# Kernel tuning notes

Measured on AMD Instinct MI355X. Metric: run time of the kernel, lower is better.

The kernel has to match this reference:

```python
import jax, jax.numpy as jnp
import numpy as np
import math

ALPHA = 0.5


def _dfrft_matrix(N: int, a: float) -> np.ndarray:
    """Candan's discrete fractional Fourier transform matrix (approx order 2),
    as used by torch-frft's dfrft. D(a) = E diag(exp(-i*pi/2*a*k)) E^T, where E
    are eigenvectors (even/odd interleaved, descending eigenvalue) of the
    S = circulant([0,1,0,...,0,1]) + diag(Re fft(s)) matrix that commutes with the DFT.
    Pure numpy; runs at trace time (constants)."""
    s = np.zeros(N)
    s[1] = 1.0
    s[-1] = 1.0
    idx = (np.arange(N)[:, None] - np.arange(N)[None, :]) % N
    S = s[idx] + np.diag(np.fft.fft(s).real)
    # odd/even decomposition matrix P (orthogonal)
    r = N // 2
    even = 1 - (N % 2)
    P = np.zeros((N, N))
    P[0, 0] = 1.0
    c = 1.0 / math.sqrt(2.0)
    for i in range(1, r - even + 1):
        P[i, i] = c
        P[i, N - i] = c
    if even:
        P[r, r] = 1.0
    for i in range(r + 1, N):
        P[i, i] = -c
        P[i, N - i] = c
    CS = P @ S @ P.T
    C2 = CS[: r + 1, : r + 1]
    S2 = CS[r + 1:, r + 1:]
    _, vc = np.linalg.eigh(C2)  # ascending -> reverse for descending order
    _, vs = np.linalg.eigh(S2)
    SC2 = (P @ np.vstack((vc, np.zeros((N - r - 1, r + 1)))))[:, ::-1]  # even evecs
    SS2 = (P @ np.vstack((np.zeros((r + 1, N - r - 1)), vs)))[:, ::-1]  # odd evecs
    if N % 2 == 0:
        E = np.zeros((N, N + 1))
        E[:, 0::2] = SC2
        E[:, 1::2] = np.hstack((SS2, np.zeros((N, 1))))
        E = np.delete(E, N - 1, axis=1)  # skip eigenvalue index N-1, keep N
    else:
        E = np.zeros((N, N))
        E[:, 0::2] = SC2
        E[:, 1::2] = SS2
    shift = 1 - (N % 2)
    k = np.concatenate((np.arange(N - 1), [N - 1 + shift]))
    f = np.exp(-1j * (np.pi / 2.0) * a * k)
    return (E * f[None, :]) @ E.T


def setup_inputs() -> dict:
    key = jax.random.key(0)
    k1, k2, k3, k4, k5 = jax.random.split(key, 5)
    B, Ci, Co, H, W = 16, 64, 64, 128, 128
    scale = 1.0 / Ci
    return {
        "x": jax.random.normal(k1, (B, Ci, H, W), jnp.float32),
        "w_r": jax.random.normal(k2, (Co, Ci), jnp.float32) * scale,
        "w_i": jax.random.normal(k3, (Co, Ci), jnp.float32) * scale,
        "b_r": jax.random.normal(k4, (Co,), jnp.float32) * scale,
        "b_i": jax.random.normal(k5, (Co,), jnp.float32) * scale,
    }


def reference(x, w_r, w_i, b_r, b_i):
    B, Ci, H, W = x.shape
    Aw = jnp.asarray(_dfrft_matrix(W, ALPHA), jnp.complex64)   # dfrft along dim=-1
    Ah = jnp.asarray(_dfrft_matrix(H, ALPHA), jnp.complex64)   # dfrft along dim=-2
    xc = x.astype(jnp.complex64)
    # forward fractional Fourier transforms
    x_ft = jnp.einsum('wv,bchv->bchw', Aw, xc)
    x_ft = jnp.einsum('hg,bcgw->bchw', Ah, x_ft)
    # 1x1 complex conv (complex weight + bias)
    wc = w_r.astype(jnp.complex64) + 1j * w_i.astype(jnp.complex64)
    bc = b_r.astype(jnp.complex64) + 1j * b_i.astype(jnp.complex64)
    out_ft = jnp.einsum('oi,bihw->bohw', wc, x_ft) + bc[None, :, None, None]
    # inverse transforms: D(-a) = conj(D(a)) since eigenvectors are real
    y = jnp.einsum('hg,bogw->bohw', jnp.conj(Ah), out_ft)
    y = jnp.einsum('wv,bohv->bohw', jnp.conj(Aw), y)
    # module returns a complex tensor; expose as stacked (real, imag)
    return jnp.stack((y.real, y.imag), axis=0)
```

## Files before the change

### kernel.cpp

```cpp
#include <hip/hip_runtime.h>
#include <cmath>
#include <cstring>
#include <vector>
#include <algorithm>


struct UV { float ur[128]; float ui[128]; };
static UV g_uv;

namespace {

constexpr int NN = 128;

void matmul_d(const std::vector<double>& A, const std::vector<double>& B,
              std::vector<double>& C, int n) {
  for (int i = 0; i < n; ++i)
    for (int j = 0; j < n; ++j) {
      double s = 0.0;
      for (int k = 0; k < n; ++k) s += A[(size_t)i*n+k] * B[(size_t)k*n+j];
      C[(size_t)i*n+j] = s;
    }
}

void jacobi_eigh(std::vector<double>& A, int n, std::vector<double>& V,
                 std::vector<double>& lam) {
  V.assign((size_t)n*n, 0.0);
  for (int i = 0; i < n; ++i) V[(size_t)i*n+i] = 1.0;
  for (int sweep = 0; sweep < 200; ++sweep) {
    double off = 0.0;
    for (int p = 0; p < n; ++p)
      for (int q = p+1; q < n; ++q) off += A[(size_t)p*n+q]*A[(size_t)p*n+q];
    if (off < 1e-24) break;
    for (int p = 0; p < n-1; ++p)
      for (int q = p+1; q < n; ++q) {
        double apq = A[(size_t)p*n+q];
        if (std::fabs(apq) < 1e-300) continue;
        double app = A[(size_t)p*n+p], aqq = A[(size_t)q*n+q];
        double tau = (aqq - app) / (2.0*apq);
        double t = (tau >= 0 ? 1.0 : -1.0) / (std::fabs(tau) + std::sqrt(1.0 + tau*tau));
        double c = 1.0/std::sqrt(1.0 + t*t), s = t*c;
        for (int k = 0; k < n; ++k) {
          double akp = A[(size_t)k*n+p], akq = A[(size_t)k*n+q];
          A[(size_t)k*n+p] = c*akp - s*akq;
          A[(size_t)k*n+q] = s*akp + c*akq;
        }
        for (int k = 0; k < n; ++k) {
          double apk = A[(size_t)p*n+k], aqk = A[(size_t)q*n+k];
          A[(size_t)p*n+k] = c*apk - s*aqk;
          A[(size_t)q*n+k] = s*apk + c*aqk;
        }
        for (int k = 0; k < n; ++k) {
          double vkp = V[(size_t)k*n+p], vkq = V[(size_t)k*n+q];
          V[(size_t)k*n+p] = c*vkp - s*vkq;
          V[(size_t)k*n+q] = s*vkp + c*vkq;
        }
      }
  }
  lam.resize(n);
  for (int i = 0; i < n; ++i) lam[i] = A[(size_t)i*n+i];
}

bool init_uv() {
  const int n = NN, r = NN/2;
  const double c = 1.0/std::sqrt(2.0);
  const double PI = 3.14159265358979323846;
  std::vector<double> S((size_t)n*n, 0.0), P((size_t)n*n, 0.0);
  for (int i = 0; i < n; ++i) {
    S[(size_t)i*n+i] = 2.0*std::cos(2.0*PI*i/n);
    S[(size_t)i*n + (i+1)%n] += 1.0;
    S[(size_t)i*n + (i-1+n)%n] += 1.0;
  }
  P[0] = 1.0;
  for (int i = 1; i <= r-1; ++i) { P[(size_t)i*n+i] = c;  P[(size_t)i*n + (n-i)] = c; }
  P[(size_t)r*n+r] = 1.0;
  for (int i = r+1; i < n; ++i)  { P[(size_t)i*n+i] = -c; P[(size_t)i*n + (n-i)] = c; }
  std::vector<double> Pt((size_t)n*n), T((size_t)n*n), CS((size_t)n*n);
  for (int i = 0; i < n; ++i)
    for (int j = 0; j < n; ++j) Pt[(size_t)i*n+j] = P[(size_t)j*n+i];
  matmul_d(P, S, T, n);
  matmul_d(T, Pt, CS, n);
  const int m = r + 1;
  std::vector<double> C2((size_t)m*m);
  for (int i = 0; i < m; ++i)
    for (int j = 0; j < m; ++j) C2[(size_t)i*m+j] = CS[(size_t)i*n+j];
  std::vector<double> V, lam;
  jacobi_eigh(C2, m, V, lam);
  std::vector<int> idx(m);
  for (int i = 0; i < m; ++i) idx[i] = i;
  std::sort(idx.begin(), idx.end(), [&](int a, int b){ return lam[a] < lam[b]; });
  double ure[NN] = {0}, uim[NN] = {0};
  for (int mm = 0; mm < m; ++mm) {
    int col = idx[m-1-mm];
    double q[NN];
    q[0] = V[(size_t)0*m+col];
    for (int j = 1; j <= r-1; ++j) q[j] = c * V[(size_t)j*m+col];
    q[r] = V[(size_t)r*m+col];
    for (int j = r+1; j < n; ++j)  q[j] = c * V[(size_t)(n-j)*m+col];
    double ssum = 0.0;
    for (int j = 0; j < n; ++j) ssum += q[j];
    switch (mm & 3) {
      case 0: for (int h = 0; h < n; ++h) ure[h] += q[h]*ssum; break;
      case 1: for (int h = 0; h < n; ++h) uim[h] += q[h]*ssum; break;
      case 2: for (int h = 0; h < n; ++h) ure[h] -= q[h]*ssum; break;
      case 3: for (int h = 0; h < n; ++h) uim[h] -= q[h]*ssum; break;
    }
  }
  for (int h = 0; h < n; ++h) { g_uv.ur[h] = (float)ure[h]; g_uv.ui[h] = (float)uim[h]; }
  return true;
}

bool g_inited = init_uv();

}


typedef const float __attribute__((address_space(1)))* gas_fp;
typedef float __attribute__((address_space(3)))* las_fp;

__global__ __launch_bounds__(256) void transpose_w_kernel(
    const float* __restrict__ wr, const float* __restrict__ wi,
    float* __restrict__ wTr, float* __restrict__ wTi) {
  int t = blockIdx.x * 256 + threadIdx.x;
  if (t < 4096) {
    int o = t >> 6, i = t & 63;
    wTr[i*64 + o] = wr[t];
    wTi[i*64 + o] = wi[t];
  }
}

__global__ __launch_bounds__(512, 4) void spec_main_kernel(
    const float* __restrict__ x,
    const float* __restrict__ wTr, const float* __restrict__ wTi,
    const float* __restrict__ br, const float* __restrict__ bi,
    float* __restrict__ out, UV uv) {
  __shared__ float xs[64][256];
  const int tid  = threadIdx.x;
  const int bid  = blockIdx.x;
  const int b    = bid >> 6;
  const int pair = bid & 63;
  const int wave = tid >> 6;
  const int lane = tid & 63;
  const int row  = lane >> 5;
  const int p4   = (lane & 31) << 2;
  const int o0   = __builtin_amdgcn_readfirstlane(wave << 3);
  const int hrow = (pair << 1) + row;
  const int loff = (row << 7) + p4;

  const float* xb = x + ((long long)b << 20) + ((long long)hrow << 7) + p4;

#pragma unroll
  for (int j = 0; j < 4; ++j) {
    int c = (wave << 2) + j;
    __builtin_amdgcn_global_load_lds((gas_fp)(xb + ((long long)c << 14)),
                                     (las_fp)&xs[c][0], 16, 0, 0);
  }
  __syncthreads();

#pragma unroll
  for (int j = 0; j < 4; ++j) {
    int c = 32 + (wave << 2) + j;
    __builtin_amdgcn_global_load_lds((gas_fp)(xb + ((long long)c << 14)),
                                     (las_fp)&xs[c][0], 16, 0, 0);
  }

  const float uhr = uv.ur[hrow], uhi = uv.ui[hrow];
  float gr[4], gi[4];
#pragma unroll
  for (int k = 0; k < 4; ++k) {
    float vr = uv.ur[p4+k], vi = uv.ui[p4+k];
    gr[k] = uhr*vr - uhi*vi;
    gi[k] = uhr*vi + uhi*vr;
  }

  float accr[8][4], acci[8][4];
#pragma unroll
  for (int oo = 0; oo < 8; ++oo) {
    float bro = br[o0+oo], bio = bi[o0+oo];
#pragma unroll
    for (int k = 0; k < 4; ++k) {
      accr[oo][k] = bro*gr[k] - bio*gi[k];
      acci[oo][k] = bro*gi[k] + bio*gr[k];
    }
  }

#pragma unroll 4
  for (int i = 0; i < 32; ++i) {
    float4 xv = *(const float4*)&xs[i][loff];
    const float* wr0 = wTr + (i << 6) + o0;
    const float* wi0 = wTi + (i << 6) + o0;
#pragma unroll
    for (int oo = 0; oo < 8; ++oo) {
      float wr = wr0[oo], wi = wi0[oo];
      accr[oo][0] += wr*xv.x;  accr[oo][1] += wr*xv.y;
      accr[oo][2] += wr*xv.z;  accr[oo][3] += wr*xv.w;
      acci[oo][0] += wi*xv.x;  acci[oo][1] += wi*xv.y;
      acci[oo][2] += wi*xv.z;  acci[oo][3] += wi*xv.w;
    }
  }
  __syncthreads();

#pragma unroll 4
  for (int i = 32; i < 64; ++i) {
    float4 xv = *(const float4*)&xs[i][loff];
    const float* wr0 = wTr + (i << 6) + o0;
    const float* wi0 = wTi + (i << 6) + o0;
#pragma unroll
    for (int oo = 0; oo < 8; ++oo) {
      float wr = wr0[oo], wi = wi0[oo];
      accr[oo][0] += wr*xv.x;  accr[oo][1] += wr*xv.y;
      accr[oo][2] += wr*xv.z;  accr[oo][3] += wr*xv.w;
      acci[oo][0] += wi*xv.x;  acci[oo][1] += wi*xv.y;
      acci[oo][2] += wi*xv.z;  acci[oo][3] += wi*xv.w;
    }
  }

  const long long posg  = ((long long)hrow << 7) + p4;
  long long baseR = ((long long)(b*64 + o0) << 14) + posg;
  long long baseI = baseR + ((long long)(16*64) << 14);
#pragma unroll
  for (int oo = 0; oo < 8; ++oo) {
    *(float4*)&out[baseR + ((long long)oo << 14)] =
        make_float4(accr[oo][0], accr[oo][1], accr[oo][2], accr[oo][3]);
    *(float4*)&out[baseI + ((long long)oo << 14)] =
        make_float4(acci[oo][0], acci[oo][1], acci[oo][2], acci[oo][3]);
  }
}

extern "C" void kernel_launch(void* const* d_in, const int* in_sizes, int n_in,
                              void* d_out, int out_size, void* d_ws, size_t ws_size,
                              hipStream_t stream) {
  (void)in_sizes; (void)n_in; (void)out_size; (void)ws_size; (void)g_inited;
  const float* x  = (const float*)d_in[0];
  const float* wr = (const float*)d_in[1];
  const float* wi = (const float*)d_in[2];
  const float* br = (const float*)d_in[3];
  const float* bi = (const float*)d_in[4];
  float* out = (float*)d_out;
  float* wTr = (float*)d_ws;
  float* wTi = wTr + 4096;

  transpose_w_kernel<<<16, 256, 0, stream>>>(wr, wi, wTr, wTi);
  spec_main_kernel<<<1024, 512, 0, stream>>>(x, wTr, wTi, br, bi, out, g_uv);
}
```

Before: 209.6 us.

## Compute channel mix with bf16 MFMA using prepacked weight fragments

```diff
diff --git a/kernel.cpp b/kernel.cpp
--- a/kernel.cpp
+++ b/kernel.cpp
@@ -116,113 +116,127 @@
 
 typedef const float __attribute__((address_space(1)))* gas_fp;
 typedef float __attribute__((address_space(3)))* las_fp;
-
-__global__ __launch_bounds__(256) void transpose_w_kernel(
+typedef __bf16 bf16x8 __attribute__((ext_vector_type(8)));
+typedef float f32x16 __attribute__((ext_vector_type(16)));
+union FW { uint4 u; bf16x8 v; };
+
+__global__ __launch_bounds__(256) void prep_kernel(
     const float* __restrict__ wr, const float* __restrict__ wi,
-    float* __restrict__ wTr, float* __restrict__ wTi) {
+    const float* __restrict__ br, const float* __restrict__ bi,
+    uint4* __restrict__ fragW, float2* __restrict__ fragB) {
   int t = blockIdx.x * 256 + threadIdx.x;
-  if (t < 4096) {
-    int o = t >> 6, i = t & 63;
-    wTr[i*64 + o] = wr[t];
-    wTi[i*64 + o] = wi[t];
+  if (t < 1024) {
+    int lane = t & 63, rest = t >> 6;
+    int p = rest & 1, ot = (rest >> 1) & 1, kk = rest >> 2;
+    const float* w = p ? wi : wr;
+    int o  = ot*32 + (lane & 31);
+    int kh = (lane >> 5) << 2;
+    unsigned short us[8];
+#pragma unroll
+    for (int j = 0; j < 8; ++j) {
+      int cch = kk*16 + kh + (j & 3) + ((j >> 2) << 3);
+      union { __bf16 h; unsigned short s; } cv;
+      cv.h = (__bf16)w[o*64 + cch];
+      us[j] = cv.s;
+    }
+    uint4 u;
+    u.x = (unsigned)us[0] | ((unsigned)us[1] << 16);
+    u.y = (unsigned)us[2] | ((unsigned)us[3] << 16);
+    u.z = (unsigned)us[4] | ((unsigned)us[5] << 16);
+    u.w = (unsigned)us[6] | ((unsigned)us[7] << 16);
+    fragW[t] = u;
+  } else if (t < 3072) {
+    int q = t - 1024;
+    int lane = q & 63, rr = q >> 6;
+    int r = rr & 15, ot = rr >> 4;
+    int o = ot*32 + (r & 3) + ((r >> 2) << 3) + ((lane >> 5) << 2);
+    fragB[q] = make_float2(br[o], bi[o]);
   }
 }
 
 __global__ __launch_bounds__(512, 4) void spec_main_kernel(
     const float* __restrict__ x,
-    const float* __restrict__ wTr, const float* __restrict__ wTi,
-    const float* __restrict__ br, const float* __restrict__ bi,
+    const uint4* __restrict__ fragW, const float2* __restrict__ fragB,
     float* __restrict__ out, UV uv) {
   __shared__ float xs[64][256];
   const int tid  = threadIdx.x;
   const int bid  = blockIdx.x;
   const int b    = bid >> 6;
   const int pair = bid & 63;
-  const int wave = tid >> 6;
+  const int wv   = tid >> 6;
   const int lane = tid & 63;
-  const int row  = lane >> 5;
+  const int hl   = lane >> 5;
   const int p4   = (lane & 31) << 2;
-  const int o0   = __builtin_amdgcn_readfirstlane(wave << 3);
-  const int hrow = (pair << 1) + row;
-  const int loff = (row << 7) + p4;
-
-  const float* xb = x + ((long long)b << 20) + ((long long)hrow << 7) + p4;
+
+  const float* xb = x + ((long long)b << 20)
+                      + ((long long)((pair << 1) + hl) << 7) + p4;
 
 #pragma unroll
   for (int j = 0; j < 4; ++j) {
-    int c = (wave << 2) + j;
+    int c = (wv << 2) + j;
     __builtin_amdgcn_global_load_lds((gas_fp)(xb + ((long long)c << 14)),
                                      (las_fp)&xs[c][0], 16, 0, 0);
   }
   __syncthreads();
-
 #pragma unroll
   for (int j = 0; j < 4; ++j) {
-    int c = 32 + (wave << 2) + j;
+    int c = 32 + (wv << 2) + j;
     __builtin_amdgcn_global_load_lds((gas_fp)(xb + ((long long)c << 14)),
                                      (las_fp)&xs[c][0], 16, 0, 0);
   }
 
-  const float uhr = uv.ur[hrow], uhi = uv.ui[hrow];
-  float gr[4], gi[4];
-#pragma unroll
-  for (int k = 0; k < 4; ++k) {
-    float vr = uv.ur[p4+k], vi = uv.ui[p4+k];
-    gr[k] = uhr*vr - uhi*vi;
-    gi[k] = uhr*vi + uhi*vr;
-  }
-
-  float accr[8][4], acci[8][4];
-#pragma unroll
-  for (int oo = 0; oo < 8; ++oo) {
-    float bro = br[o0+oo], bio = bi[o0+oo];
-#pragma unroll
-    for (int k = 0; k < 4; ++k) {
-      accr[oo][k] = bro*gr[k] - bio*gi[k];
-      acci[oo][k] = bro*gi[k] + bio*gr[k];
-    }
-  }
-
-#pragma unroll 4
-  for (int i = 0; i < 32; ++i) {
-    float4 xv = *(const float4*)&xs[i][loff];
-    const float* wr0 = wTr + (i << 6) + o0;
-    const float* wi0 = wTi + (i << 6) + o0;
-#pragma unroll
-    for (int oo = 0; oo < 8; ++oo) {
-      float wr = wr0[oo], wi = wi0[oo];
-      accr[oo][0] += wr*xv.x;  accr[oo][1] += wr*xv.y;
-      accr[oo][2] += wr*xv.z;  accr[oo][3] += wr*xv.w;
-      acci[oo][0] += wi*xv.x;  acci[oo][1] += wi*xv.y;
-      acci[oo][2] += wi*xv.z;  acci[oo][3] += wi*xv.w;
-    }
-  }
+  const int p = (wv << 5) + (lane & 31);
+
+  f32x16 zero;
+#pragma unroll
+  for (int i = 0; i < 16; ++i) zero[i] = 0.0f;
+  f32x16 aR0 = zero, aI0 = zero, aR1 = zero, aI1 = zero;
+
+  auto kstep = [&](int kk) {
+    bf16x8 bv;
+#pragma unroll
+    for (int j = 0; j < 8; ++j) {
+      int cch = kk*16 + (hl << 2) + (j & 3) + ((j >> 2) << 3);
+      bv[j] = (__bf16)xs[cch][p];
+    }
+    const int base = (kk << 8);
+    FW a0, a1, a2, a3;
+    a0.u = fragW[base       + lane];
+    a1.u = fragW[base +  64 + lane];
+    a2.u = fragW[base + 128 + lane];
+    a3.u = fragW[base + 192 + lane];
+    aR0 = __builtin_amdgcn_mfma_f32_32x32x16_bf16(a0.v, bv, aR0, 0, 0, 0);
+    aI0 = __builtin_amdgcn_mfma_f32_32x32x16_bf16(a1.v, bv, aI0, 0, 0, 0);
+    aR1 = __builtin_amdgcn_mfma_f32_32x32x16_bf16(a2.v, bv, aR1, 0, 0, 0);
+    aI1 = __builtin_amdgcn_mfma_f32_32x32x16_bf16(a3.v, bv, aI1, 0, 0, 0);
+  };
+
+  kstep(0); kstep(1);
   __syncthreads();
-
-#pragma unroll 4
-  for (int i = 32; i < 64; ++i) {
-    float4 xv = *(const float4*)&xs[i][loff];
-    const float* wr0 = wTr + (i << 6) + o0;
-    const float* wi0 = wTi + (i << 6) + o0;
-#pragma unroll
-    for (int oo = 0; oo < 8; ++oo) {
-      float wr = wr0[oo], wi = wi0[oo];
-      accr[oo][0] += wr*xv.x;  accr[oo][1] += wr*xv.y;
-      accr[oo][2] += wr*xv.z;  accr[oo][3] += wr*xv.w;
-      acci[oo][0] += wi*xv.x;  acci[oo][1] += wi*xv.y;
-      acci[oo][2] += wi*xv.z;  acci[oo][3] += wi*xv.w;
-    }
-  }
-
-  const long long posg  = ((long long)hrow << 7) + p4;
-  long long baseR = ((long long)(b*64 + o0) << 14) + posg;
-  long long baseI = baseR + ((long long)(16*64) << 14);
-#pragma unroll
-  for (int oo = 0; oo < 8; ++oo) {
-    *(float4*)&out[baseR + ((long long)oo << 14)] =
-        make_float4(accr[oo][0], accr[oo][1], accr[oo][2], accr[oo][3]);
-    *(float4*)&out[baseI + ((long long)oo << 14)] =
-        make_float4(acci[oo][0], acci[oo][1], acci[oo][2], acci[oo][3]);
+  kstep(2); kstep(3);
+
+  const int wcol = p & 127;
+  const int h    = (pair << 1) + (p >> 7);
+  const float uhr = uv.ur[h],    uhi = uv.ui[h];
+  const float vr  = uv.ur[wcol], vi  = uv.ui[wcol];
+  const float gr = uhr*vr - uhi*vi, gi = uhr*vi + uhi*vr;
+
+  const long long base = ((long long)(b * 64) << 14) + ((long long)pair << 8) + p;
+#pragma unroll
+  for (int r = 0; r < 16; ++r) {
+    float2 bc = fragB[(r << 6) + lane];
+    int o = (r & 3) + ((r >> 2) << 3) + (hl << 2);
+    long long off = base + ((long long)o << 14);
+    out[off]             = aR0[r] + bc.x*gr - bc.y*gi;
+    out[off + (1 << 24)] = aI0[r] + bc.x*gi + bc.y*gr;
+  }
+#pragma unroll
+  for (int r = 0; r < 16; ++r) {
+    float2 bc = fragB[((16 + r) << 6) + lane];
+    int o = 32 + (r & 3) + ((r >> 2) << 3) + (hl << 2);
+    long long off = base + ((long long)o << 14);
+    out[off]             = aR1[r] + bc.x*gr - bc.y*gi;
+    out[off + (1 << 24)] = aI1[r] + bc.x*gi + bc.y*gr;
   }
 }
 
@@ -236,9 +250,9 @@
   const float* br = (const float*)d_in[3];
   const float* bi = (const float*)d_in[4];
   float* out = (float*)d_out;
-  float* wTr = (float*)d_ws;
-  float* wTi = wTr + 4096;
-
-  transpose_w_kernel<<<16, 256, 0, stream>>>(wr, wi, wTr, wTi);
-  spec_main_kernel<<<1024, 512, 0, stream>>>(x, wTr, wTi, br, bi, out, g_uv);
-}
+  uint4*  fragW = (uint4*)d_ws;
+  float2* fragB = (float2*)((char*)d_ws + 16384);
+
+  prep_kernel<<<12, 256, 0, stream>>>(wr, wi, br, bi, fragW, fragB);
+  spec_main_kernel<<<1024, 512, 0, stream>>>(x, fragW, fragB, out, g_uv);
+}
```

After: 194.0 us. 7.4% less time.
